# Performance work log

Hardware: AMD Instinct MI355X
Metric: run time of the kernel (lower is better)

Reference implementation:

```python
import jax, jax.numpy as jnp
import numpy as np

B, S, P, D, H, R = 2, 2048, 1024, 2048, 16, 16
DH = D // H  # 128


def _rope(t, cos, sin):
    # t: [B,S,H,DH]; cos/sin: [S, DH//2]; complex pair rotation
    t2 = t.reshape(t.shape[0], t.shape[1], t.shape[2], DH // 2, 2)
    a, b = t2[..., 0], t2[..., 1]
    c = cos[None, :, None, :]
    s = sin[None, :, None, :]
    out = jnp.stack([a * c - b * s, a * s + b * c], axis=-1)
    return out.reshape(t.shape)


def setup_inputs() -> dict:
    key = jax.random.key(0)
    ks = jax.random.split(key, 16)
    sc = 1.0 / np.sqrt(D)
    inv_freq = 1.0 / (10000.0 ** (np.arange(0, DH, 2, dtype=np.float32) / DH))
    pos = (P + np.arange(S, dtype=np.float32))[:, None] * inv_freq[None, :]
    i_idx = np.arange(S)[:, None]
    j_idx = np.arange(P + S)[None, :]
    mask = np.where(j_idx <= P + i_idx, 0.0, -1e9).astype(np.float32)
    return {
        "x": jax.random.normal(ks[0], (B, S, D), jnp.float32),
        "freqs_cos": jnp.asarray(np.cos(pos)),
        "freqs_sin": jnp.asarray(np.sin(pos)),
        "mask": jnp.asarray(mask)[None, None],
        "prev_key": jax.random.normal(ks[1], (B, P, H, DH), jnp.float32),
        "prev_value": jax.random.normal(ks[2], (B, P, H, DH), jnp.float32),
        "pooled_scale": jax.random.uniform(ks[3], (B, 1), jnp.float32),
        "wq": jax.random.normal(ks[4], (D, D), jnp.float32) * sc,
        "wk": jax.random.normal(ks[5], (D, D), jnp.float32) * sc,
        "wv": jax.random.normal(ks[6], (D, D), jnp.float32) * sc,
        "wo": jax.random.normal(ks[7], (D, D), jnp.float32) * sc,
        "wq_A": jax.random.normal(ks[8], (D, R), jnp.float32) * sc,
        "wq_B": jax.random.normal(ks[9], (R, D), jnp.float32) * 0.02,
        "wk_A": jax.random.normal(ks[10], (D, R), jnp.float32) * sc,
        "wk_B": jax.random.normal(ks[11], (R, D), jnp.float32) * 0.02,
        "wv_A": jax.random.normal(ks[12], (D, R), jnp.float32) * sc,
        "wv_B": jax.random.normal(ks[13], (R, D), jnp.float32) * 0.02,
        "wo_A": jax.random.normal(ks[14], (D, R), jnp.float32) * sc,
        "wo_B": jax.random.normal(ks[15], (R, D), jnp.float32) * 0.02,
    }


def reference(x, freqs_cos, freqs_sin, mask, prev_key, prev_value, pooled_scale,
              wq, wk, wv, wo, wq_A, wq_B, wk_A, wk_B, wv_A, wv_B, wo_A, wo_B):
    ps = pooled_scale[:, None, :]  # [B,1,1] per-batch LoRA scale
    xq = x @ wq.T + (x @ wq_A) @ wq_B * ps
    xk = x @ wk.T + (x @ wk_A) @ wk_B * ps
    xv = x @ wv.T + (x @ wv_A) @ wv_B * ps
    xq = xq.reshape(B, S, H, DH)
    xk = xk.reshape(B, S, H, DH)
    xv = xv.reshape(B, S, H, DH)
    xq = _rope(xq, freqs_cos, freqs_sin)
    xk = _rope(xk, freqs_cos, freqs_sin)
    keys = jnp.concatenate([prev_key, xk], axis=1)      # [B,P+S,H,DH]
    values = jnp.concatenate([prev_value, xv], axis=1)
    q = xq.transpose(0, 2, 1, 3)       # [B,H,S,DH]
    k = keys.transpose(0, 2, 1, 3)     # [B,H,P+S,DH]
    v = values.transpose(0, 2, 1, 3)
    scores = jnp.einsum("bhqd,bhkd->bhqk", q, k) / jnp.sqrt(jnp.float32(DH))
    scores = scores + mask
    probs = jax.nn.softmax(scores.astype(jnp.float32), axis=-1).astype(q.dtype)
    out = jnp.einsum("bhqk,bhkd->bhqd", probs, v)
    out = out.transpose(0, 2, 1, 3).reshape(B, S, D)
    return out @ wo.T + (out @ wo_A) @ wo_B * ps
```

## Files before the change

### kernel.cpp

```cpp
#include <hip/hip_runtime.h>
#include <stdint.h>

#define BB 2
#define SS 2048
#define PP 1024
#define DD 2048
#define HH 16
#define RR 16
#define DHH 128
#define TT (PP + SS)
#define BSR (BB * SS)

typedef __attribute__((ext_vector_type(8))) _Float16 half8;
typedef __attribute__((ext_vector_type(4))) float f32x4;

typedef __attribute__((address_space(3))) unsigned int lds_uint;
typedef const __attribute__((address_space(1))) unsigned int glb_uint;
__device__ __forceinline__ void async_copy16(const void* g, void* l) {
    __builtin_amdgcn_global_load_lds((glb_uint*)g, (lds_uint*)l, 16, 0, 0);
}

__global__ __launch_bounds__(256) void cvt_f16_kernel(
    const float* __restrict__ in, _Float16* __restrict__ out, int n4)
{
    int idx = blockIdx.x * 256 + threadIdx.x;
    int stride = gridDim.x * 256;
    for (int c = idx; c < n4; c += stride) {
        float4 v = *(const float4*)(in + (size_t)c * 4);
        union { _Float16 h[4]; uint2 u; } o;
        o.h[0] = (_Float16)v.x; o.h[1] = (_Float16)v.y;
        o.h[2] = (_Float16)v.z; o.h[3] = (_Float16)v.w;
        *(uint2*)(out + (size_t)c * 4) = o.u;
    }
}

__global__ __launch_bounds__(256) void lora_t_kernel(
    const float* __restrict__ A,
    const float* __restrict__ w0, const float* __restrict__ w1,
    const float* __restrict__ w2,
    float* __restrict__ tout)
{
    const float* wA = (blockIdx.z == 0) ? w0 : (blockIdx.z == 1) ? w1 : w2;
    int i  = blockIdx.x * 16 + (threadIdx.x >> 4);
    int r  = threadIdx.x & 15;
    int k0 = blockIdx.y * 512;
    const float* arow = A  + (size_t)i  * DD + k0;
    const float* wcol = wA + (size_t)k0 * RR + r;
    float acc = 0.f;
#pragma unroll 4
    for (int k = 0; k < 512; ++k)
        acc += arow[k] * wcol[k * RR];
    atomicAdd(&tout[(size_t)blockIdx.z * (BSR * RR) + (size_t)i * RR + r], acc);
}

__global__ __launch_bounds__(256) void lora_t_f16_kernel(
    const _Float16* __restrict__ A, const float* __restrict__ wA,
    float* __restrict__ tout)
{
    int i  = blockIdx.x * 16 + (threadIdx.x >> 4);
    int r  = threadIdx.x & 15;
    int k0 = blockIdx.y * 512;
    const _Float16* arow = A + (size_t)i * DD + k0;
    const float* wcol = wA + (size_t)k0 * RR + r;
    float acc = 0.f;
#pragma unroll 4
    for (int k = 0; k < 512; ++k)
        acc += (float)arow[k] * wcol[k * RR];
    atomicAdd(&tout[(size_t)i * RR + r], acc);
}

__global__ __launch_bounds__(256, 3) void gemm_f16_kernel(
    const _Float16* __restrict__ Ah, const _Float16* __restrict__ Wh,
    float* __restrict__ o0, float* __restrict__ o1, float* __restrict__ o2)
{
    __shared__ __align__(16) _Float16 As[128 * 32];
    __shared__ __align__(16) _Float16 Bs[128 * 32];
    const int tid  = threadIdx.x;
    const int wv   = tid >> 6;
    const int lane = tid & 63;
    const int ln   = lane & 15;
    const int quad = lane >> 4;
    const int i0   = blockIdx.x * 128;
    const int j0f  = blockIdx.y * 128;
    const int mat  = j0f >> 11;
    const int jloc = j0f & 2047;
    float* out_f = (mat == 0) ? o0 : (mat == 1) ? o1 : o2;
    const int mb   = (wv >> 1) * 4;
    const int nb   = (wv & 1) * 4;
    const int srow = wv * 32 + (lane >> 2);
    const int scol = (lane & 3) * 8;

    f32x4 zero = {0.f, 0.f, 0.f, 0.f};
    f32x4 acc[4][4];
#pragma unroll
    for (int a = 0; a < 4; ++a)
#pragma unroll
        for (int c = 0; c < 4; ++c) acc[a][c] = zero;

    const _Float16* gA = Ah + (size_t)(i0 + srow) * DD + scol;
    const _Float16* gB = Wh + (size_t)(j0f + srow) * DD + scol;
    _Float16* lA0 = As + (wv * 32) * 32;
    _Float16* lA1 = As + (wv * 32 + 16) * 32;
    _Float16* lB0 = Bs + (wv * 32) * 32;
    _Float16* lB1 = Bs + (wv * 32 + 16) * 32;

    for (int k0 = 0; k0 < DD; k0 += 32) {
        async_copy16(gA + k0, lA0);
        async_copy16(gA + (size_t)16 * DD + k0, lA1);
        async_copy16(gB + k0, lB0);
        async_copy16(gB + (size_t)16 * DD + k0, lB1);
        __syncthreads();
        half8 b[4];
#pragma unroll
        for (int nt = 0; nt < 4; ++nt)
            b[nt] = *(const half8*)&Bs[((nb + nt) * 16 + ln) * 32 + quad * 8];
#pragma unroll
        for (int mt = 0; mt < 4; ++mt) {
            half8 a = *(const half8*)&As[((mb + mt) * 16 + ln) * 32 + quad * 8];
#pragma unroll
            for (int nt = 0; nt < 4; ++nt)
                acc[mt][nt] = __builtin_amdgcn_mfma_f32_16x16x32_f16(a, b[nt], acc[mt][nt], 0, 0, 0);
        }
        __syncthreads();
    }

#pragma unroll
    for (int mt = 0; mt < 4; ++mt)
#pragma unroll
        for (int nt = 0; nt < 4; ++nt)
#pragma unroll
            for (int reg = 0; reg < 4; ++reg) {
                int row = i0 + (mb + mt) * 16 + quad * 4 + reg;
                int col = jloc + (nb + nt) * 16 + ln;
                out_f[(size_t)row * DD + col] = acc[mt][nt][reg];
            }
}

__global__ __launch_bounds__(256) void lora_add_kernel(
    const float* __restrict__ t, const float* __restrict__ wB,
    const float* __restrict__ ps, float* __restrict__ out)
{
    const int n4 = BSR * (DD / 4);
    int idx = blockIdx.x * 256 + threadIdx.x;
    int stride = gridDim.x * 256;
    for (int c = idx; c < n4; c += stride) {
        int i  = c >> 9;
        int j4 = c & 511;
        float psb = ps[i >> 11];
        const float* trow = t + (size_t)i * RR;
        float* op = out + (size_t)i * DD + j4 * 4;
        f32x4 acc = *(const f32x4*)op;
#pragma unroll
        for (int r = 0; r < 16; ++r) {
            float tv = psb * trow[r];
            f32x4 w = *(const f32x4*)(wB + (size_t)r * DD + j4 * 4);
#pragma unroll
            for (int q = 0; q < 4; ++q)
                acc[q] += tv * w[q];
        }
        *(f32x4*)op = acc;
    }
}

__global__ __launch_bounds__(256) void prev_scatter_kernel(
    const float* __restrict__ pk, const float* __restrict__ pv,
    _Float16* __restrict__ kh, _Float16* __restrict__ vTh)
{
    __shared__ __align__(16) _Float16 vt[128][72];
    const int pt = blockIdx.x, h = blockIdx.y;
    const int b = pt >> 4, p0 = (pt & 15) * 64;
    const int tid = threadIdx.x;
    const size_t bh = (size_t)(b * HH + h);
#pragma unroll
    for (int p = 0; p < 8; ++p) {
        int c = tid + 256 * p;
        int pl = c >> 5, c4 = (c & 31) * 4;
        float4 v4 = *(const float4*)(pk + (((size_t)(b * PP + p0 + pl)) * HH + h) * DHH + c4);
        union { _Float16 h4[4]; uint2 u; } o;
        o.h4[0] = (_Float16)v4.x; o.h4[1] = (_Float16)v4.y;
        o.h4[2] = (_Float16)v4.z; o.h4[3] = (_Float16)v4.w;
        *(uint2*)(kh + (bh * TT + p0 + pl) * DHH + c4) = o.u;
    }
#pragma unroll
    for (int p = 0; p < 8; ++p) {
        int c = tid + 256 * p;
        int pl = c >> 5, c4 = (c & 31) * 4;
        float4 v4 = *(const float4*)(pv + (((size_t)(b * PP + p0 + pl)) * HH + h) * DHH + c4);
        vt[c4 + 0][pl] = (_Float16)v4.x;
        vt[c4 + 1][pl] = (_Float16)v4.y;
        vt[c4 + 2][pl] = (_Float16)v4.z;
        vt[c4 + 3][pl] = (_Float16)v4.w;
    }
    __syncthreads();
#pragma unroll
    for (int p = 0; p < 4; ++p) {
        int c = tid + 256 * p;
        int d = c >> 3, c8 = (c & 7) * 8;
        *(half8*)(vTh + (bh * DHH + d) * TT + p0 + c8) = *(const half8*)&vt[d][c8];
    }
}

__global__ __launch_bounds__(256) void rope_scatter_kernel(
    const float* __restrict__ xq, const float* __restrict__ xk,
    const float* __restrict__ xv,
    const float* __restrict__ t_all,
    const float* __restrict__ wqB, const float* __restrict__ wkB,
    const float* __restrict__ wvB,
    const float* __restrict__ ps,
    const float* __restrict__ fcos, const float* __restrict__ fsin,
    _Float16* __restrict__ qh, _Float16* __restrict__ kh,
    _Float16* __restrict__ vTh)
{
    __shared__ float tS[64][48];
    __shared__ float wBs[3][16][128];
    __shared__ __align__(16) _Float16 vt[128][72];
    const int st = blockIdx.x, h = blockIdx.y;
    const int i0 = st * 64;
    const int b  = i0 >> 11;
    const int s0 = i0 & 2047;
    const int tid = threadIdx.x;
    const size_t bh = (size_t)(b * HH + h);
    const float QSC = 0.12753102f;

#pragma unroll
    for (int p = 0; p < 12; ++p) {
        int idx = tid + 256 * p;
        int w = idx >> 10, rem = idx & 1023;
        int sl = rem >> 4, r = rem & 15;
        tS[sl][w * 16 + r] = t_all[(size_t)w * (BSR * RR) + (size_t)(i0 + sl) * RR + r];
    }
#pragma unroll
    for (int w = 0; w < 3; ++w) {
        const float* src = (w == 0) ? wqB : (w == 1) ? wkB : wvB;
#pragma unroll
        for (int p = 0; p < 8; ++p) {
            int idx = tid + 256 * p;
            int r = idx >> 7, dd = idx & 127;
            wBs[w][r][dd] = src[(size_t)r * DD + h * DHH + dd];
        }
    }
    __syncthreads();
    const float psb = ps[b];

#pragma unroll
    for (int w = 0; w < 2; ++w) {
        const float* src = (w == 0) ? xq : xk;
        for (int p = 0; p < 16; ++p) {
            int pp = tid + 256 * p;
            int sl = pp >> 6, dd = pp & 63;
            int d = dd * 2;
            int i = i0 + sl, s = s0 + sl;
            float2 pr = *(const float2*)(src + (size_t)i * DD + h * DHH + d);
            float a = pr.x, b2 = pr.y;
            float la = 0.f, lb = 0.f;
#pragma unroll
            for (int r = 0; r < 16; ++r) {
                float tv = tS[sl][w * 16 + r];
                la += tv * wBs[w][r][d];
                lb += tv * wBs[w][r][d + 1];
            }
            a  += psb * la;
            b2 += psb * lb;
            float c  = fcos[(size_t)s * 64 + dd];
            float sn = fsin[(size_t)s * 64 + dd];
            float na = a * c - b2 * sn;
            float nb = a * sn + b2 * c;
            union { _Float16 h2[2]; unsigned u; } o;
            if (w == 0) {
                o.h2[0] = (_Float16)(na * QSC); o.h2[1] = (_Float16)(nb * QSC);
                *(unsigned*)(qh + (bh * SS + s) * DHH + d) = o.u;
            } else {
                o.h2[0] = (_Float16)na; o.h2[1] = (_Float16)nb;
                *(unsigned*)(kh + (bh * TT + PP + s) * DHH + d) = o.u;
            }
        }
    }
    for (int p = 0; p < 16; ++p) {
        int pp = tid + 256 * p;
        int sl = pp >> 6, dd = pp & 63;
        int d = dd * 2;
        int i = i0 + sl;
        float2 pr = *(const float2*)(xv + (size_t)i * DD + h * DHH + d);
        float a = pr.x, b2 = pr.y;
        float la = 0.f, lb = 0.f;
#pragma unroll
        for (int r = 0; r < 16; ++r) {
            float tv = tS[sl][32 + r];
            la += tv * wBs[2][r][d];
            lb += tv * wBs[2][r][d + 1];
        }
        a  += psb * la;
        b2 += psb * lb;
        vt[d][sl]     = (_Float16)a;
        vt[d + 1][sl] = (_Float16)b2;
    }
    __syncthreads();
#pragma unroll
    for (int p = 0; p < 4; ++p) {
        int c = tid + 256 * p;
        int d = c >> 3, c8 = (c & 7) * 8;
        *(half8*)(vTh + (bh * DHH + d) * TT + PP + s0 + c8) = *(const half8*)&vt[d][c8];
    }
}

__global__ __launch_bounds__(256) void attn_kernel(
    const _Float16* __restrict__ qh, const _Float16* __restrict__ kh,
    const _Float16* __restrict__ vTh, _Float16* __restrict__ attn_h,
    float* __restrict__ pbuf, float* __restrict__ lbuf)
{
    __shared__ __align__(16) _Float16 k_lds[64][136];
    __shared__ __align__(16) _Float16 v_lds[128][72];
    __shared__ __align__(16) _Float16 p_lds[4][2][16][72];
    const int lin = blockIdx.x;
    const int s   = lin >> 8;
    const int r5  = lin & 255;
    const int bh_i = r5 & 31;
    const int q8   = r5 >> 5;
    const int h = bh_i & 15, b = bh_i >> 4;
    int qt, t0, t1, ntf;
    if (s == 0) { qt = q8;      ntf = 18 + 2 * q8; t0 = 0; t1 = ntf; }
    else {
        qt = 15 - q8; ntf = 48 - 2 * q8;
        int mid = (24 - q8) & ~1;
        if (s == 1) { t0 = 0;   t1 = mid; }
        else        { t0 = mid; t1 = ntf; }
    }
    const bool partial = (s != 0);
    const int qbase = qt * 128;
    const int tid = threadIdx.x, wv = tid >> 6, lane = tid & 63;
    const int ln = lane & 15, quad = lane >> 4;
    const size_t bh = (size_t)(b * HH + h);

    half8 qfrag[2][4];
#pragma unroll
    for (int mt = 0; mt < 2; ++mt) {
        const _Float16* qrow = qh + (bh * SS + qbase + wv * 32 + mt * 16 + ln) * DHH;
#pragma unroll
        for (int ks = 0; ks < 4; ++ks)
            qfrag[mt][ks] = *(const half8*)(qrow + ks * 32 + quad * 8);
    }
    f32x4 zero = {0.f, 0.f, 0.f, 0.f};
    f32x4 O[2][8];
#pragma unroll
    for (int mt = 0; mt < 2; ++mt)
#pragma unroll
        for (int i = 0; i < 8; ++i) O[mt][i] = zero;
    float l_part[2][4];
#pragma unroll
    for (int mt = 0; mt < 2; ++mt)
#pragma unroll
        for (int r = 0; r < 4; ++r) l_part[mt][r] = 0.f;

    int offKg[4], offKl[4], offVg[4], offVl[4];
#pragma unroll
    for (int p = 0; p < 4; ++p) {
        int c = tid + 256 * p;
        int key = c >> 4, ck = (c & 15) * 8;
        offKg[p] = key * DHH + ck;
        offKl[p] = key * 136 + ck;
        int d = c >> 3, cv = (c & 7) * 8;
        offVg[p] = d * TT + cv;
        offVl[p] = d * 72 + cv;
    }
    const _Float16* kbase = kh + bh * (size_t)TT * DHH;
    const _Float16* vbase = vTh + bh * (size_t)DHH * TT;

    half8 k0r[4], v0r[4], k1r[4], v1r[4];
    {
        const _Float16* kg0 = kbase + (size_t)(t0 * 64) * DHH;
        const _Float16* vg0 = vbase + t0 * 64;
#pragma unroll
        for (int p = 0; p < 4; ++p) {
            k0r[p] = *(const half8*)(kg0 + offKg[p]);
            v0r[p] = *(const half8*)(vg0 + offVg[p]);
        }
    }

#define ATTN_BODY(KT, KC, VC, KN, VN)                                          \
  {                                                                            \
    const int kb = (KT) * 64;                                                  \
    _Pragma("unroll")                                                          \
    for (int p = 0; p < 4; ++p) {                                              \
        *(half8*)((_Float16*)k_lds + offKl[p]) = KC[p];                        \
        *(half8*)((_Float16*)v_lds + offVl[p]) = VC[p];                        \
    }                                                                          \
    __syncthreads();                                                           \
    if ((KT) + 1 < t1) {                                                       \
        const _Float16* kg = kbase + (size_t)(kb + 64) * DHH;                  \
        const _Float16* vg = vbase + (kb + 64);                                \
        _Pragma("unroll")                                                      \
        for (int p = 0; p < 4; ++p) {                                          \
            KN[p] = *(const half8*)(kg + offKg[p]);                            \
            VN[p] = *(const half8*)(vg + offVg[p]);                            \
        }                                                                      \
    }                                                                          \
    f32x4 sv[2][4];                                                            \
    __builtin_amdgcn_s_setprio(1);                                             \
    _Pragma("unroll")                                                          \
    for (int nt = 0; nt < 4; ++nt) {                                           \
        half8 kf[4];                                                           \
        _Pragma("unroll")                                                      \
        for (int ks = 0; ks < 4; ++ks)                                         \
            kf[ks] = *(const half8*)&k_lds[nt * 16 + ln][ks * 32 + quad * 8];  \
        _Pragma("unroll")                                                      \
        for (int mt = 0; mt < 2; ++mt) {                                       \
            f32x4 sacc = zero;                                                 \
            _Pragma("unroll")                                                  \
            for (int ks = 0; ks < 4; ++ks)                                     \
                sacc = __builtin_amdgcn_mfma_f32_16x16x32_f16(qfrag[mt][ks], kf[ks], sacc, 0, 0, 0); \
            sv[mt][nt] = sacc;                                                 \
        }                                                                      \
    }                                                                          \
    __builtin_amdgcn_s_setprio(0);                                             \
    const bool tail = ((KT) >= ntf - 2);                                       \
    _Pragma("unroll")                                                          \
    for (int mt = 0; mt < 2; ++mt)                                             \
        _Pragma("unroll")                                                      \
        for (int nt = 0; nt < 4; ++nt)                                         \
            _Pragma("unroll")                                                  \
            for (int reg = 0; reg < 4; ++reg) {                                \
                float z = sv[mt][nt][reg];                                     \
                if (tail) {                                                    \
                    int jj = kb + nt * 16 + ln;                                \
                    int rg = PP + qbase + wv * 32 + mt * 16 + quad * 4 + reg;  \
                    if (jj > rg) z = -1e30f;                                   \
                }                                                              \
                float pz = exp2f(z - 12.f);                                    \
                l_part[mt][reg] += pz;                                         \
                {                                                              \
                    int row = quad * 4 + reg;                                  \
                    int cs  = (nt * 2 + (ln >> 3)) ^ ((row >> 1) & 7);         \
                    p_lds[wv][mt][row][cs * 8 + (ln & 7)] = (_Float16)pz;      \
                }                                                              \
            }                                                                  \
    __builtin_amdgcn_s_setprio(1);                                             \
    _Pragma("unroll")                                                          \
    for (int kf2 = 0; kf2 < 2; ++kf2) {                                        \
        int cA = ((kf2 * 4 + quad) ^ ((ln >> 1) & 7)) * 8;                     \
        half8 pa0 = *(const half8*)&p_lds[wv][0][ln][cA];                      \
        half8 pa1 = *(const half8*)&p_lds[wv][1][ln][cA];                      \
        _Pragma("unroll")                                                      \
        for (int d8 = 0; d8 < 8; ++d8) {                                       \
            half8 vb = *(const half8*)&v_lds[d8 * 16 + ln][kf2 * 32 + quad * 8]; \
            O[0][d8] = __builtin_amdgcn_mfma_f32_16x16x32_f16(pa0, vb, O[0][d8], 0, 0, 0); \
            O[1][d8] = __builtin_amdgcn_mfma_f32_16x16x32_f16(pa1, vb, O[1][d8], 0, 0, 0); \
        }                                                                      \
    }                                                                          \
    __builtin_amdgcn_s_setprio(0);                                             \
    __syncthreads();                                                           \
  }

    for (int kt = t0; kt < t1; kt += 2) {
        ATTN_BODY(kt,     k0r, v0r, k1r, v1r);
        ATTN_BODY(kt + 1, k1r, v1r, k0r, v0r);
    }
#undef ATTN_BODY

#pragma unroll
    for (int mt = 0; mt < 2; ++mt)
#pragma unroll
        for (int reg = 0; reg < 4; ++reg) {
            float l = l_part[mt][reg];
#pragma unroll
            for (int off = 1; off < 16; off <<= 1)
                l += __shfl_xor(l, off);
            l_part[mt][reg] = l;
        }

    if (!partial) {
#pragma unroll
        for (int mt = 0; mt < 2; ++mt)
#pragma unroll
            for (int d8 = 0; d8 < 8; ++d8)
#pragma unroll
                for (int reg = 0; reg < 4; ++reg) {
                    int row = qbase + wv * 32 + mt * 16 + quad * 4 + reg;
                    int col = h * DHH + d8 * 16 + ln;
                    attn_h[((size_t)b * SS + row) * DD + col] =
                        (_Float16)(O[mt][d8][reg] / l_part[mt][reg]);
                }
    } else {
        const int chunkid = r5 * 2 + (s - 1);
        float* pb = pbuf + (size_t)chunkid * (128 * 128);
        float* lb = lbuf + (size_t)chunkid * 128;
#pragma unroll
        for (int mt = 0; mt < 2; ++mt)
#pragma unroll
            for (int reg = 0; reg < 4; ++reg)
                if (ln == 0)
                    lb[wv * 32 + mt * 16 + quad * 4 + reg] = l_part[mt][reg];
#pragma unroll
        for (int mt = 0; mt < 2; ++mt)
#pragma unroll
            for (int d8 = 0; d8 < 8; ++d8)
#pragma unroll
                for (int reg = 0; reg < 4; ++reg) {
                    int row = wv * 32 + mt * 16 + quad * 4 + reg;
                    pb[(size_t)row * 128 + d8 * 16 + ln] = O[mt][d8][reg];
                }
    }
}

__global__ __launch_bounds__(256) void attn_combine_kernel(
    const float* __restrict__ pbuf, const float* __restrict__ lbuf,
    _Float16* __restrict__ attn_h)
{
    const int r5 = blockIdx.x;
    const int bh_i = r5 & 31, q8 = r5 >> 5;
    const int h = bh_i & 15, b = bh_i >> 4;
    const int qt = 15 - q8, qbase = qt * 128;
    const int tid = threadIdx.x;
    const int row = tid >> 1, c0 = (tid & 1) * 64;
    const float* pa = pbuf + (size_t)(r5 * 2) * (128 * 128) + (size_t)row * 128 + c0;
    const float* pbv = pa + 128 * 128;
    float inv = 1.f / (lbuf[(size_t)(r5 * 2) * 128 + row] +
                       lbuf[(size_t)(r5 * 2 + 1) * 128 + row]);
    _Float16* orow = attn_h + ((size_t)b * SS + qbase + row) * DD + h * DHH + c0;
#pragma unroll
    for (int j = 0; j < 64; j += 4) {
        float4 va = *(const float4*)(pa + j);
        float4 vb = *(const float4*)(pbv + j);
        union { _Float16 h4[4]; uint2 u; } o;
        o.h4[0] = (_Float16)((va.x + vb.x) * inv);
        o.h4[1] = (_Float16)((va.y + vb.y) * inv);
        o.h4[2] = (_Float16)((va.z + vb.z) * inv);
        o.h4[3] = (_Float16)((va.w + vb.w) * inv);
        *(uint2*)(orow + j) = o.u;
    }
}

extern "C" void kernel_launch(void* const* d_in, const int* in_sizes, int n_in,
                              void* d_out, int out_size, void* d_ws, size_t ws_size,
                              hipStream_t stream) {
    const float* x    = (const float*)d_in[0];
    const float* fcos = (const float*)d_in[1];
    const float* fsin = (const float*)d_in[2];
    const float* pk   = (const float*)d_in[4];
    const float* pv   = (const float*)d_in[5];
    const float* ps   = (const float*)d_in[6];
    const float* wq   = (const float*)d_in[7];
    const float* wk   = (const float*)d_in[8];
    const float* wvw  = (const float*)d_in[9];
    const float* wo   = (const float*)d_in[10];
    const float* wqA  = (const float*)d_in[11];
    const float* wqB  = (const float*)d_in[12];
    const float* wkA  = (const float*)d_in[13];
    const float* wkB  = (const float*)d_in[14];
    const float* wvA  = (const float*)d_in[15];
    const float* wvB  = (const float*)d_in[16];
    const float* woA  = (const float*)d_in[17];
    const float* woB  = (const float*)d_in[18];
    float* out = (float*)d_out;

    float* t_all = (float*)d_ws;
    float* t_o   = t_all + 3 * BSR * RR;
    float* xq    = t_all + 4 * BSR * RR;
    float* xk    = xq + (size_t)BSR * DD;
    float* xv    = xk + (size_t)BSR * DD;
    _Float16* xh    = (_Float16*)(xv + (size_t)BSR * DD);
    _Float16* wqkvh = xh + (size_t)BSR * DD;
    _Float16* woh   = wqkvh + (size_t)3 * DD * DD;
    _Float16* qh_   = woh + (size_t)DD * DD;
    _Float16* kh_   = qh_ + (size_t)BB * HH * SS * DHH;
    _Float16* vTh   = kh_ + (size_t)BB * HH * TT * DHH;
    _Float16* attn_h = vTh + (size_t)BB * HH * DHH * TT;
    float* pbuf = xq;
    float* lbuf = xk;
    (void)ws_size; (void)in_sizes; (void)n_in; (void)out_size;

    hipMemsetAsync(t_all, 0, (size_t)4 * BSR * RR * sizeof(float), stream);

    cvt_f16_kernel<<<512, 256, 0, stream>>>(x,   xh, (BSR * DD) / 4);
    cvt_f16_kernel<<<512, 256, 0, stream>>>(wq,  wqkvh,                       (DD * DD) / 4);
    cvt_f16_kernel<<<512, 256, 0, stream>>>(wk,  wqkvh + (size_t)DD * DD,     (DD * DD) / 4);
    cvt_f16_kernel<<<512, 256, 0, stream>>>(wvw, wqkvh + (size_t)2 * DD * DD, (DD * DD) / 4);
    cvt_f16_kernel<<<512, 256, 0, stream>>>(wo,  woh, (DD * DD) / 4);

    lora_t_kernel<<<dim3(256, 4, 3), 256, 0, stream>>>(x, wqA, wkA, wvA, t_all);

    gemm_f16_kernel<<<dim3(32, 48), 256, 0, stream>>>(xh, wqkvh, xq, xk, xv);

    prev_scatter_kernel<<<dim3(32, 16), 256, 0, stream>>>(pk, pv, kh_, vTh);

    rope_scatter_kernel<<<dim3(64, 16), 256, 0, stream>>>(xq, xk, xv, t_all,
                                                          wqB, wkB, wvB, ps,
                                                          fcos, fsin,
                                                          qh_, kh_, vTh);

    attn_kernel<<<768, 256, 0, stream>>>(qh_, kh_, vTh, attn_h, pbuf, lbuf);

    attn_combine_kernel<<<256, 256, 0, stream>>>(pbuf, lbuf, attn_h);

    lora_t_f16_kernel<<<dim3(256, 4), 256, 0, stream>>>(attn_h, woA, t_o);

    gemm_f16_kernel<<<dim3(32, 16), 256, 0, stream>>>(attn_h, woh, out, out, out);

    lora_add_kernel<<<2048, 256, 0, stream>>>(t_o, woB, ps, out);
}
```

Baseline: 785.2 us.

## Alias attention K and P tiles in one LDS buffer and batch fp16 conversions

The attention kernel now shares one LDS array between the K tile and the per-wave probability tile, with an extra barrier after the score computation so P can overwrite K. This cuts LDS per block, which should let more blocks fit per CU. The cost is an added __syncthreads per key tile and holding probabilities in registers longer. Separately, the five fp32-to-fp16 conversion launches are merged into a single launch with a 2D grid to cut launch overhead.

```diff
diff --git a/kernel.cpp b/kernel.cpp
--- a/kernel.cpp
+++ b/kernel.cpp
@@ -20,9 +20,24 @@
     __builtin_amdgcn_global_load_lds((glb_uint*)g, (lds_uint*)l, 16, 0, 0);
 }
 
-__global__ __launch_bounds__(256) void cvt_f16_kernel(
-    const float* __restrict__ in, _Float16* __restrict__ out, int n4)
-{
+__global__ __launch_bounds__(256) void cvt_f16x5_kernel(
+    const float* __restrict__ s0, const float* __restrict__ s1,
+    const float* __restrict__ s2, const float* __restrict__ s3,
+    const float* __restrict__ s4,
+    _Float16* __restrict__ dx, _Float16* __restrict__ dqkv,
+    _Float16* __restrict__ dwo)
+{
+    const int seg = blockIdx.y;
+    const float* in;
+    _Float16* out;
+    int n4;
+    if (seg == 0)      { in = s0; out = dx;  n4 = (BSR * DD) / 4; }
+    else if (seg == 4) { in = s4; out = dwo; n4 = (DD * DD) / 4; }
+    else {
+        in  = (seg == 1) ? s1 : (seg == 2) ? s2 : s3;
+        out = dqkv + (size_t)(seg - 1) * DD * DD;
+        n4  = (DD * DD) / 4;
+    }
     int idx = blockIdx.x * 256 + threadIdx.x;
     int stride = gridDim.x * 256;
     for (int c = idx; c < n4; c += stride) {
@@ -308,9 +323,8 @@
     const _Float16* __restrict__ vTh, _Float16* __restrict__ attn_h,
     float* __restrict__ pbuf, float* __restrict__ lbuf)
 {
-    __shared__ __align__(16) _Float16 k_lds[64][136];
+    __shared__ __align__(16) _Float16 U[64][152];
     __shared__ __align__(16) _Float16 v_lds[128][72];
-    __shared__ __align__(16) _Float16 p_lds[4][2][16][72];
     const int lin = blockIdx.x;
     const int s   = lin >> 8;
     const int r5  = lin & 255;
@@ -357,7 +371,7 @@
         int c = tid + 256 * p;
         int key = c >> 4, ck = (c & 15) * 8;
         offKg[p] = key * DHH + ck;
-        offKl[p] = key * 136 + ck;
+        offKl[p] = key * 152 + ck;
         int d = c >> 3, cv = (c & 7) * 8;
         offVg[p] = d * TT + cv;
         offVl[p] = d * 72 + cv;
@@ -381,7 +395,7 @@
     const int kb = (KT) * 64;                                                  \
     _Pragma("unroll")                                                          \
     for (int p = 0; p < 4; ++p) {                                              \
-        *(half8*)((_Float16*)k_lds + offKl[p]) = KC[p];                        \
+        *(half8*)((_Float16*)U + offKl[p]) = KC[p];                            \
         *(half8*)((_Float16*)v_lds + offVl[p]) = VC[p];                        \
     }                                                                          \
     __syncthreads();                                                           \
@@ -401,7 +415,7 @@
         half8 kf[4];                                                           \
         _Pragma("unroll")                                                      \
         for (int ks = 0; ks < 4; ++ks)                                         \
-            kf[ks] = *(const half8*)&k_lds[nt * 16 + ln][ks * 32 + quad * 8];  \
+            kf[ks] = *(const half8*)&U[nt * 16 + ln][ks * 32 + quad * 8];      \
         _Pragma("unroll")                                                      \
         for (int mt = 0; mt < 2; ++mt) {                                       \
             f32x4 sacc = zero;                                                 \
@@ -427,18 +441,26 @@
                 }                                                              \
                 float pz = exp2f(z - 12.f);                                    \
                 l_part[mt][reg] += pz;                                         \
-                {                                                              \
-                    int row = quad * 4 + reg;                                  \
-                    int cs  = (nt * 2 + (ln >> 3)) ^ ((row >> 1) & 7);         \
-                    p_lds[wv][mt][row][cs * 8 + (ln & 7)] = (_Float16)pz;      \
-                }                                                              \
+                sv[mt][nt][reg] = pz;                                          \
+            }                                                                  \
+    __syncthreads();         \
+    _Pragma("unroll")                                                          \
+    for (int mt = 0; mt < 2; ++mt)                                             \
+        _Pragma("unroll")                                                      \
+        for (int nt = 0; nt < 4; ++nt)                                         \
+            _Pragma("unroll")                                                  \
+            for (int reg = 0; reg < 4; ++reg) {                                \
+                int row = quad * 4 + reg;                                      \
+                int cs  = (nt * 2 + (ln >> 3)) ^ ((row >> 1) & 7);             \
+                U[wv * 16 + row][mt * 72 + cs * 8 + (ln & 7)] =                \
+                    (_Float16)sv[mt][nt][reg];                                 \
             }                                                                  \
     __builtin_amdgcn_s_setprio(1);                                             \
     _Pragma("unroll")                                                          \
     for (int kf2 = 0; kf2 < 2; ++kf2) {                                        \
         int cA = ((kf2 * 4 + quad) ^ ((ln >> 1) & 7)) * 8;                     \
-        half8 pa0 = *(const half8*)&p_lds[wv][0][ln][cA];                      \
-        half8 pa1 = *(const half8*)&p_lds[wv][1][ln][cA];                      \
+        half8 pa0 = *(const half8*)&U[wv * 16 + ln][cA];                       \
+        half8 pa1 = *(const half8*)&U[wv * 16 + ln][72 + cA];                  \
         _Pragma("unroll")                                                      \
         for (int d8 = 0; d8 < 8; ++d8) {                                       \
             half8 vb = *(const half8*)&v_lds[d8 * 16 + ln][kf2 * 32 + quad * 8]; \
@@ -447,7 +469,7 @@
         }                                                                      \
     }                                                                          \
     __builtin_amdgcn_s_setprio(0);                                             \
-    __syncthreads();                                                           \
+    __syncthreads();        \
   }
 
     for (int kt = t0; kt < t1; kt += 2) {
@@ -570,11 +592,8 @@
 
     hipMemsetAsync(t_all, 0, (size_t)4 * BSR * RR * sizeof(float), stream);
 
-    cvt_f16_kernel<<<512, 256, 0, stream>>>(x,   xh, (BSR * DD) / 4);
-    cvt_f16_kernel<<<512, 256, 0, stream>>>(wq,  wqkvh,                       (DD * DD) / 4);
-    cvt_f16_kernel<<<512, 256, 0, stream>>>(wk,  wqkvh + (size_t)DD * DD,     (DD * DD) / 4);
-    cvt_f16_kernel<<<512, 256, 0, stream>>>(wvw, wqkvh + (size_t)2 * DD * DD, (DD * DD) / 4);
-    cvt_f16_kernel<<<512, 256, 0, stream>>>(wo,  woh, (DD * DD) / 4);
+    cvt_f16x5_kernel<<<dim3(512, 5), 256, 0, stream>>>(x, wq, wk, wvw, wo,
+                                                       xh, wqkvh, woh);
 
     lora_t_kernel<<<dim3(256, 4, 3), 256, 0, stream>>>(x, wqA, wkA, wvA, t_all);
 
```

Measured after the change: 793.6 us. About the same (+1.1%).
